# Kernel tuning notes

Hardware: AMD Instinct MI355X
Metric: run time of the kernel (lower is better)

The kernel has to match this reference:

```python
import jax, jax.numpy as jnp
import numpy as np

ALPHA = 0.9
EPS = 1e-5
SEQ, BATCH, D_MODEL, FF_DIM = 2048, 16, 512, 2048


def _layer_norm(x, g, b):
    m = jnp.mean(x, axis=-1, keepdims=True)
    v = jnp.mean((x - m) ** 2, axis=-1, keepdims=True)
    return (x - m) * jax.lax.rsqrt(v + EPS) * g + b


def _decay_matrix(seq, dtype):
    # Closed form of the torch roll/flip/tril loop:
    #   W[i, j] = alpha^{i-j+1}            for j <= i
    #   W[i, i] += 1 - sum_{k=1}^{i+1} alpha^k   (diag correction)
    i = jnp.arange(seq)
    diff = i[:, None] - i[None, :]                       # [S, S]
    causal = diff >= 0
    expo = jnp.where(causal, diff + 1, 0).astype(dtype)
    W = jnp.where(causal, jnp.asarray(ALPHA, dtype) ** expo, 0.0)
    W = W + jnp.diag(1.0 - W.sum(axis=1))
    return W


def setup_inputs() -> dict:
    key = jax.random.key(0)
    ks = jax.random.split(key, 8)
    s = lambda fan: 1.0 / np.sqrt(fan)
    return {
        "x": jax.random.normal(ks[0], (SEQ, BATCH, D_MODEL), jnp.float32),
        "w_lin": jax.random.normal(ks[1], (D_MODEL, D_MODEL), jnp.float32) * s(D_MODEL),
        "b_lin": jax.random.normal(ks[2], (D_MODEL,), jnp.float32) * 0.01,
        "w1": jax.random.normal(ks[3], (FF_DIM, D_MODEL), jnp.float32) * s(D_MODEL),
        "b1": jax.random.normal(ks[4], (FF_DIM,), jnp.float32) * 0.01,
        "w2": jax.random.normal(ks[5], (D_MODEL, FF_DIM), jnp.float32) * s(FF_DIM),
        "b2": jax.random.normal(ks[6], (D_MODEL,), jnp.float32) * 0.01,
        "g1": jnp.ones((D_MODEL,), jnp.float32),
        "beta1": jnp.zeros((D_MODEL,), jnp.float32),
        "g2": jnp.ones((D_MODEL,), jnp.float32),
        "beta2": jnp.zeros((D_MODEL,), jnp.float32),
    }


def reference(x, w_lin, b_lin, w1, b1, w2, b2, g1, beta1, g2, beta2):
    seq = x.shape[0]
    W = _decay_matrix(seq, x.dtype)                      # [S, S]

    # attention sublayer (dropout = identity in eval)
    y = _layer_norm(x, g1, beta1)
    z = jnp.einsum("sbd,ed->sbe", y, w_lin) + b_lin       # projection
    attn = jnp.einsum("ih,hbd->ibd", W, z)                # causal exp-decay mixing
    x = x + attn

    # feed-forward sublayer
    y = _layer_norm(x, g2, beta2)
    h = jax.nn.relu(jnp.einsum("sbd,fd->sbf", y, w1) + b1)
    ff = jnp.einsum("sbf,df->sbd", h, w2) + b2
    return x + ff
```

## Files before the change

### kernel.cpp

```cpp
#include <hip/hip_runtime.h>

#define SEQ 2048
#define BATCH 16
#define DMODEL 512
#define FFDIM 2048
#define NTOK (SEQ * BATCH)
#define ALPHA 0.9f

typedef unsigned short u16;
typedef __attribute__((ext_vector_type(8))) short short8;
typedef __attribute__((ext_vector_type(4))) float f32x4;

__device__ __forceinline__ float bf2f(u16 u) {
    unsigned int v = ((unsigned int)u) << 16;
    return __builtin_bit_cast(float, v);
}
__device__ __forceinline__ u16 f2bf(float f) {
    unsigned int v = __builtin_bit_cast(unsigned int, f);
    v += 0x7fffu + ((v >> 16) & 1u);
    return (u16)(v >> 16);
}

__global__ __launch_bounds__(256) void cvt_kernel(const float* __restrict__ in,
                                                  u16* __restrict__ out, int n) {
    const int i = (blockIdx.x * 256 + threadIdx.x) * 4;
    if (i >= n) return;
    float4 v = *(const float4*)(in + i);
    ushort4 o;
    o.x = f2bf(v.x); o.y = f2bf(v.y); o.z = f2bf(v.z); o.w = f2bf(v.w);
    *(ushort4*)(out + i) = o;
}

__global__ __launch_bounds__(256) void ln_kernel(const float* __restrict__ xin,
                                                 const float* __restrict__ g,
                                                 const float* __restrict__ b,
                                                 u16* __restrict__ y) {
    const int lane = threadIdx.x & 63;
    const int wave = threadIdx.x >> 6;
    const long tok = (long)blockIdx.x * 4 + wave;
    const long off = tok * DMODEL + lane * 8;

    float f[8];
    {
        const float4* xp = (const float4*)(xin + off);
        float4 a = xp[0], c = xp[1];
        f[0] = a.x; f[1] = a.y; f[2] = a.z; f[3] = a.w;
        f[4] = c.x; f[5] = c.y; f[6] = c.z; f[7] = c.w;
    }
    float s = 0.f, s2 = 0.f;
#pragma unroll
    for (int i = 0; i < 8; i++) { s += f[i]; s2 += f[i] * f[i]; }
#pragma unroll
    for (int o = 32; o > 0; o >>= 1) {
        s += __shfl_xor(s, o, 64);
        s2 += __shfl_xor(s2, o, 64);
    }
    const float mean = s * (1.f / DMODEL);
    const float var = s2 * (1.f / DMODEL) - mean * mean;
    const float inv = rsqrtf(var + 1e-5f);

    const float4* gp = (const float4*)(g + lane * 8);
    const float4* bp = (const float4*)(b + lane * 8);
    float4 g0 = gp[0], g1 = gp[1], b0 = bp[0], b1 = bp[1];
    float gg[8] = {g0.x, g0.y, g0.z, g0.w, g1.x, g1.y, g1.z, g1.w};
    float bb[8] = {b0.x, b0.y, b0.z, b0.w, b1.x, b1.y, b1.z, b1.w};
    short8 ov;
#pragma unroll
    for (int i = 0; i < 8; i++)
        ov[i] = (short)f2bf((f[i] - mean) * inv * gg[i] + bb[i]);
    *(short8*)(y + off) = ov;
}

#define SCAN_L 128
#define SCAN_H 160
__global__ __launch_bounds__(256) void scan_kernel(const u16* __restrict__ z,
                                                   const float* __restrict__ x,
                                                   float* __restrict__ x1) {
    const int p = blockIdx.x * 256 + threadIdx.x;
    const int s0 = blockIdx.y * SCAN_L;
    int s = s0 - SCAN_H;
    if (s < 0) s = 0;
    float r = 0.f;
    for (; s < s0; ++s)
        r = ALPHA * (bf2f(z[(long)s * 8192 + p]) + r);

    float ap = powf(ALPHA, (float)(s0 + 2));
#pragma unroll 4
    for (int i = 0; i < SCAN_L; i++) {
        const long idx = (long)(s0 + i) * 8192 + p;
        const float zf = bf2f(z[idx]);
        r = ALPHA * (zf + r);
        const float c = 1.f - (ALPHA - ap) * 10.f;
        x1[idx] = x[idx] + r + c * zf;
        ap *= ALPHA;
    }
}

#define BM 128
#define BN 128
#define BKK 64

typedef __attribute__((address_space(1))) unsigned int as1_u32;
typedef __attribute__((address_space(3))) unsigned int as3_u32;

__device__ __forceinline__ void gld_lds16(const void* g, const void* l) {
    __builtin_amdgcn_global_load_lds((as1_u32*)(unsigned long long)g,
                                     (as3_u32*)(unsigned int)(unsigned long long)l,
                                     16, 0, 0);
}

template <int EPI, bool OUT_F32>
__global__ __launch_bounds__(256, 2) void gemm128(const u16* __restrict__ A,
                                                  const u16* __restrict__ Bt,
                                                  const float* __restrict__ bias,
                                                  const float* __restrict__ resid,
                                                  void* __restrict__ C,
                                                  int M, int N, int K) {
    __shared__ alignas(16) u16 sA[2][BM * BKK];
    __shared__ alignas(16) u16 sB[2][BN * BKK];

    const int tid = threadIdx.x;
    const int lane = tid & 63;
    const int wave = tid >> 6;
    const int wr = wave >> 1;
    const int wc = wave & 1;
    const int l15 = lane & 15, q16 = lane >> 4;

    const int gx = gridDim.x;
    const int nwg = gx * gridDim.y;
    const int lin = blockIdx.y * gx + blockIdx.x;
    const int cpx = nwg >> 3;
    const int swz = (lin & 7) * cpx + (lin >> 3);
    const int m0 = (swz % gx) * BM;
    const int n0 = (swz / gx) * BN;

    const u16* gA[4];
    const u16* gB[4];
    int ldsoff[4];
#pragma unroll
    for (int i = 0; i < 4; i++) {
        const int ch = tid + i * 256;
        const int r = ch >> 3;
        const int oo = (ch & 7) ^ (r & 7);
        gA[i] = A + (long)(m0 + r) * K + oo * 8;
        gB[i] = Bt + (long)(n0 + r) * K + oo * 8;
        ldsoff[i] = ch * 8;
    }

    const int x7 = l15 & 7;
    int octk[2];
    octk[0] = ((0 + q16) ^ x7) * 8;
    octk[1] = ((4 + q16) ^ x7) * 8;
    const int rowA0 = wr * 64 + l15;
    const int rowB0 = wc * 64 + l15;

    f32x4 acc[4][4];
#pragma unroll
    for (int i = 0; i < 4; i++)
#pragma unroll
        for (int j = 0; j < 4; j++) acc[i][j] = (f32x4){0.f, 0.f, 0.f, 0.f};

    const int NT = K / BKK;

#pragma unroll
    for (int i = 0; i < 4; i++) gld_lds16(gA[i], &sA[0][ldsoff[i]]);
#pragma unroll
    for (int i = 0; i < 4; i++) gld_lds16(gB[i], &sB[0][ldsoff[i]]);

#pragma unroll 1
    for (int t = 0; t < NT; ++t) {
        const int pb = t & 1;
        if (t + 1 < NT) {
            const int pn = (t + 1) & 1;
            const int ko = (t + 1) * BKK;
#pragma unroll
            for (int i = 0; i < 4; i++) gld_lds16(gA[i] + ko, &sA[pn][ldsoff[i]]);
#pragma unroll
            for (int i = 0; i < 4; i++) gld_lds16(gB[i] + ko, &sB[pn][ldsoff[i]]);
            asm volatile("s_waitcnt vmcnt(8)" ::: "memory");
        } else {
            asm volatile("s_waitcnt vmcnt(0)" ::: "memory");
        }
        __builtin_amdgcn_s_barrier();

        const u16* pa = &sA[pb][rowA0 * BKK];
        const u16* pbb = &sB[pb][rowB0 * BKK];

#pragma unroll
        for (int kk = 0; kk < 2; kk++) {
            short8 a[4], b[4];
#pragma unroll
            for (int i = 0; i < 4; i++)
                a[i] = *(const short8*)(pa + i * 16 * BKK + octk[kk]);
#pragma unroll
            for (int j = 0; j < 4; j++)
                b[j] = *(const short8*)(pbb + j * 16 * BKK + octk[kk]);
#pragma unroll
            for (int i = 0; i < 4; i++)
#pragma unroll
                for (int j = 0; j < 4; j++)
                    acc[i][j] = __builtin_amdgcn_mfma_f32_16x16x32_bf16(a[i], b[j],
                                                                        acc[i][j], 0, 0, 0);
        }
        __builtin_amdgcn_s_barrier();
    }

#pragma unroll
    for (int i = 0; i < 4; i++) {
        const int row0 = m0 + wr * 64 + i * 16 + q16 * 4;
#pragma unroll
        for (int j = 0; j < 4; j++) {
            const int col = n0 + wc * 64 + j * 16 + l15;
            const float bv = bias[col];
#pragma unroll
            for (int r = 0; r < 4; r++) {
                const long idx = (long)(row0 + r) * N + col;
                float v = acc[i][j][r] + bv;
                if (EPI == 1) v = fmaxf(v, 0.f);
                if (EPI == 2) v += resid[idx];
                if (OUT_F32)
                    ((float*)C)[idx] = v;
                else
                    ((u16*)C)[idx] = f2bf(v);
            }
        }
    }
}

extern "C" void kernel_launch(void* const* d_in, const int* in_sizes, int n_in,
                              void* d_out, int out_size, void* d_ws, size_t ws_size,
                              hipStream_t stream) {
    const float* x = (const float*)d_in[0];
    const float* w_lin = (const float*)d_in[1];
    const float* b_lin = (const float*)d_in[2];
    const float* w1 = (const float*)d_in[3];
    const float* b1 = (const float*)d_in[4];
    const float* w2 = (const float*)d_in[5];
    const float* b2 = (const float*)d_in[6];
    const float* g1 = (const float*)d_in[7];
    const float* be1 = (const float*)d_in[8];
    const float* g2 = (const float*)d_in[9];
    const float* be2 = (const float*)d_in[10];
    float* out = (float*)d_out;

    char* ws = (char*)d_ws;
    const size_t MB = 1024 * 1024;
    u16* y = (u16*)(ws);
    float* x1 = (float*)(ws + 32 * MB);
    u16* h = (u16*)(ws + 96 * MB);
    u16* z = h;
    u16* wb_lin = (u16*)(ws + 224 * MB);
    u16* wb1 = (u16*)(ws + 225 * MB);
    u16* wb2 = (u16*)(ws + 228 * MB);

    cvt_kernel<<<(DMODEL * DMODEL) / 1024, 256, 0, stream>>>(w_lin, wb_lin, DMODEL * DMODEL);
    cvt_kernel<<<(FFDIM * DMODEL) / 1024, 256, 0, stream>>>(w1, wb1, FFDIM * DMODEL);
    cvt_kernel<<<(DMODEL * FFDIM) / 1024, 256, 0, stream>>>(w2, wb2, DMODEL * FFDIM);

    ln_kernel<<<NTOK / 4, 256, 0, stream>>>(x, g1, be1, y);
    gemm128<0, false><<<dim3(NTOK / BM, DMODEL / BN), 256, 0, stream>>>(y, wb_lin, b_lin, nullptr,
                                                                       z, NTOK, DMODEL, DMODEL);
    scan_kernel<<<dim3(BATCH * DMODEL / 256, SEQ / SCAN_L), 256, 0, stream>>>(z, x, x1);
    ln_kernel<<<NTOK / 4, 256, 0, stream>>>(x1, g2, be2, y);
    gemm128<1, false><<<dim3(NTOK / BM, FFDIM / BN), 256, 0, stream>>>(y, wb1, b1, nullptr, h,
                                                                      NTOK, FFDIM, DMODEL);
    gemm128<2, true><<<dim3(NTOK / BM, DMODEL / BN), 256, 0, stream>>>(h, wb2, b2, x1, out,
                                                                      NTOK, DMODEL, FFDIM);
}
```

Before: 456.6 us.

## Fuse decay scan with second LayerNorm and reorder GEMM tile swizzle

Merges the exponential-decay scan and the second LayerNorm into one kernel. Each block now owns one batch row's full 512-wide vector, processes two columns per thread, and does a block reduction per sequence step, so x1 is not re-read by a separate LN pass. The scan loop also gains 4-deep register prefetching of z and x. Separately, the GEMM workgroup-to-tile mapping is switched to an N-fastest order to change L2 reuse. The cost is a barrier per time step inside the scan, and the grid shrinks to 16x16 blocks, which may hurt latency hiding.

```diff
diff --git a/kernel.cpp b/kernel.cpp
--- a/kernel.cpp
+++ b/kernel.cpp
@@ -8,6 +8,7 @@
 #define ALPHA 0.9f
 
 typedef unsigned short u16;
+typedef unsigned int u32;
 typedef __attribute__((ext_vector_type(8))) short short8;
 typedef __attribute__((ext_vector_type(4))) float f32x4;
 
@@ -73,26 +74,88 @@
 
 #define SCAN_L 128
 #define SCAN_H 160
-__global__ __launch_bounds__(256) void scan_kernel(const u16* __restrict__ z,
-                                                   const float* __restrict__ x,
-                                                   float* __restrict__ x1) {
-    const int p = blockIdx.x * 256 + threadIdx.x;
+__global__ __launch_bounds__(256) void scan_ln_kernel(const u16* __restrict__ z,
+                                                      const float* __restrict__ x,
+                                                      const float* __restrict__ g,
+                                                      const float* __restrict__ be,
+                                                      float* __restrict__ x1,
+                                                      u16* __restrict__ y) {
+    __shared__ float red[2][4][2];
+    const int t = threadIdx.x;
+    const int lane = t & 63, wave = t >> 6;
+    const int b = blockIdx.x;
     const int s0 = blockIdx.y * SCAN_L;
-    int s = s0 - SCAN_H;
-    if (s < 0) s = 0;
-    float r = 0.f;
-    for (; s < s0; ++s)
-        r = ALPHA * (bf2f(z[(long)s * 8192 + p]) + r);
-
+    const int d0 = 2 * t;
+
+    const u32* zp = (const u32*)z;
+    const float2* xp = (const float2*)x;
+    float2* x1p = (float2*)x1;
+    u32* yp = (u32*)y;
+    const int colu = b * 256 + t;
+
+    const float gg0 = g[d0], gg1 = g[d0 + 1];
+    const float bb0 = be[d0], bb1 = be[d0 + 1];
+
+    float r0 = 0.f, r1 = 0.f;
+    {
+        int s = s0 - SCAN_H;
+        if (s < 0) s = 0;
+        for (; s < s0; ++s) {
+            const u32 zz = zp[(long)s * 4096 + colu];
+            r0 = ALPHA * (bf2f((u16)(zz & 0xffffu)) + r0);
+            r1 = ALPHA * (bf2f((u16)(zz >> 16)) + r1);
+        }
+    }
     float ap = powf(ALPHA, (float)(s0 + 2));
+
+    u32 zq[4];
+    float2 xq[4];
+#pragma unroll
+    for (int j = 0; j < 4; j++) {
+        zq[j] = zp[(long)(s0 + j) * 4096 + colu];
+        xq[j] = xp[(long)(s0 + j) * 4096 + colu];
+    }
+
 #pragma unroll 4
     for (int i = 0; i < SCAN_L; i++) {
-        const long idx = (long)(s0 + i) * 8192 + p;
-        const float zf = bf2f(z[idx]);
-        r = ALPHA * (zf + r);
+        const int sl = i & 3;
+        const u32 zz = zq[sl];
+        const float2 xx = xq[sl];
+        if (i + 4 < SCAN_L) {
+            zq[sl] = zp[(long)(s0 + i + 4) * 4096 + colu];
+            xq[sl] = xp[(long)(s0 + i + 4) * 4096 + colu];
+        }
+        const float z0 = bf2f((u16)(zz & 0xffffu));
+        const float z1 = bf2f((u16)(zz >> 16));
+        r0 = ALPHA * (z0 + r0);
+        r1 = ALPHA * (z1 + r1);
         const float c = 1.f - (ALPHA - ap) * 10.f;
-        x1[idx] = x[idx] + r + c * zf;
         ap *= ALPHA;
+        const float v0 = xx.x + r0 + c * z0;
+        const float v1 = xx.y + r1 + c * z1;
+        x1p[(long)(s0 + i) * 4096 + colu] = (float2){v0, v1};
+
+        float s1 = v0 + v1, s2 = v0 * v0 + v1 * v1;
+#pragma unroll
+        for (int o = 32; o > 0; o >>= 1) {
+            s1 += __shfl_xor(s1, o, 64);
+            s2 += __shfl_xor(s2, o, 64);
+        }
+        const int slot = i & 1;
+        if (lane == 0) {
+            red[slot][wave][0] = s1;
+            red[slot][wave][1] = s2;
+        }
+        asm volatile("s_waitcnt lgkmcnt(0)" ::: "memory");
+        __builtin_amdgcn_s_barrier();
+        const float S = red[slot][0][0] + red[slot][1][0] + red[slot][2][0] + red[slot][3][0];
+        const float S2 = red[slot][0][1] + red[slot][1][1] + red[slot][2][1] + red[slot][3][1];
+        const float mean = S * (1.f / DMODEL);
+        const float var = S2 * (1.f / DMODEL) - mean * mean;
+        const float inv = rsqrtf(var + 1e-5f);
+        const u16 o0 = f2bf((v0 - mean) * inv * gg0 + bb0);
+        const u16 o1 = f2bf((v1 - mean) * inv * gg1 + bb1);
+        yp[(long)(s0 + i) * 4096 + colu] = ((u32)o1 << 16) | (u32)o0;
     }
 }
 
@@ -126,13 +189,13 @@
     const int wc = wave & 1;
     const int l15 = lane & 15, q16 = lane >> 4;
 
-    const int gx = gridDim.x;
-    const int nwg = gx * gridDim.y;
-    const int lin = blockIdx.y * gx + blockIdx.x;
+    const int gy = gridDim.y;
+    const int nwg = gridDim.x * gy;
+    const int lin = blockIdx.x * gy + blockIdx.y;
     const int cpx = nwg >> 3;
     const int swz = (lin & 7) * cpx + (lin >> 3);
-    const int m0 = (swz % gx) * BM;
-    const int n0 = (swz / gx) * BN;
+    const int m0 = (swz / gy) * BM;
+    const int n0 = (swz % gy) * BN;
 
     const u16* gA[4];
     const u16* gB[4];
@@ -260,8 +323,7 @@
     ln_kernel<<<NTOK / 4, 256, 0, stream>>>(x, g1, be1, y);
     gemm128<0, false><<<dim3(NTOK / BM, DMODEL / BN), 256, 0, stream>>>(y, wb_lin, b_lin, nullptr,
                                                                        z, NTOK, DMODEL, DMODEL);
-    scan_kernel<<<dim3(BATCH * DMODEL / 256, SEQ / SCAN_L), 256, 0, stream>>>(z, x, x1);
-    ln_kernel<<<NTOK / 4, 256, 0, stream>>>(x1, g2, be2, y);
+    scan_ln_kernel<<<dim3(BATCH, SEQ / SCAN_L), 256, 0, stream>>>(z, x, g2, be2, x1, y);
     gemm128<1, false><<<dim3(NTOK / BM, FFDIM / BN), 256, 0, stream>>>(y, wb1, b1, nullptr, h,
                                                                       NTOK, FFDIM, DMODEL);
     gemm128<2, true><<<dim3(NTOK / BM, DMODEL / BN), 256, 0, stream>>>(h, wb2, b2, x1, out,
```

After: 506.0 us. 1.11x slower.

## Vectorize and prefetch scan over column pairs, shrink chunks, remap GEMM tile order

Applied to the files above, without the earlier changes.

The decay scan now handles two adjacent columns per thread, using 32-bit bf16-pair loads and float2 loads and stores, and keeps a 4-deep register prefetch queue so load latency overlaps the serial recurrence. The chunk length and warm-up halo are shortened (64/128), which gives more parallel blocks. The cost is more redundant warm-up work per output. The GEMM workgroup swizzle now assigns tiles M-major with N as the fast index, so neighbouring workgroups share A tiles in cache.

```diff
diff --git a/kernel.cpp b/kernel.cpp
--- a/kernel.cpp
+++ b/kernel.cpp
@@ -8,6 +8,7 @@
 #define ALPHA 0.9f
 
 typedef unsigned short u16;
+typedef unsigned int u32;
 typedef __attribute__((ext_vector_type(8))) short short8;
 typedef __attribute__((ext_vector_type(4))) float f32x4;
 
@@ -71,28 +72,67 @@
     *(short8*)(y + off) = ov;
 }
 
-#define SCAN_L 128
-#define SCAN_H 160
+#define SCAN_L 64
+#define SCAN_H 128
+#define NCOLU (BATCH * DMODEL / 2)
 __global__ __launch_bounds__(256) void scan_kernel(const u16* __restrict__ z,
                                                    const float* __restrict__ x,
                                                    float* __restrict__ x1) {
-    const int p = blockIdx.x * 256 + threadIdx.x;
+    const int colu = blockIdx.x * 256 + threadIdx.x;
     const int s0 = blockIdx.y * SCAN_L;
-    int s = s0 - SCAN_H;
-    if (s < 0) s = 0;
-    float r = 0.f;
-    for (; s < s0; ++s)
-        r = ALPHA * (bf2f(z[(long)s * 8192 + p]) + r);
+
+    const u32* zp = (const u32*)z;
+    const float2* xp = (const float2*)x;
+    float2* x1p = (float2*)x1;
+
+    float r0 = 0.f, r1 = 0.f;
+
+    {
+        int sb = s0 - SCAN_H;
+        if (sb < 0) sb = 0;
+        const int nw = s0 - sb;
+        if (nw > 0) {
+            u32 zq[4];
+#pragma unroll
+            for (int j = 0; j < 4; j++) zq[j] = zp[(long)(sb + j) * NCOLU + colu];
+            for (int i = 0; i < nw; i += 4) {
+#pragma unroll
+                for (int j = 0; j < 4; j++) {
+                    const u32 zz = zq[j];
+                    if (i + j + 4 < nw)
+                        zq[j] = zp[(long)(sb + i + j + 4) * NCOLU + colu];
+                    r0 = ALPHA * (bf2f((u16)(zz & 0xffffu)) + r0);
+                    r1 = ALPHA * (bf2f((u16)(zz >> 16)) + r1);
+                }
+            }
+        }
+    }
 
     float ap = powf(ALPHA, (float)(s0 + 2));
+
+    u32 zq[4];
+    float2 xq[4];
+#pragma unroll
+    for (int j = 0; j < 4; j++) {
+        zq[j] = zp[(long)(s0 + j) * NCOLU + colu];
+        xq[j] = xp[(long)(s0 + j) * NCOLU + colu];
+    }
 #pragma unroll 4
     for (int i = 0; i < SCAN_L; i++) {
-        const long idx = (long)(s0 + i) * 8192 + p;
-        const float zf = bf2f(z[idx]);
-        r = ALPHA * (zf + r);
+        const int sl = i & 3;
+        const u32 zz = zq[sl];
+        const float2 xx = xq[sl];
+        if (i + 4 < SCAN_L) {
+            zq[sl] = zp[(long)(s0 + i + 4) * NCOLU + colu];
+            xq[sl] = xp[(long)(s0 + i + 4) * NCOLU + colu];
+        }
+        const float z0 = bf2f((u16)(zz & 0xffffu));
+        const float z1 = bf2f((u16)(zz >> 16));
+        r0 = ALPHA * (z0 + r0);
+        r1 = ALPHA * (z1 + r1);
         const float c = 1.f - (ALPHA - ap) * 10.f;
-        x1[idx] = x[idx] + r + c * zf;
         ap *= ALPHA;
+        x1p[(long)(s0 + i) * NCOLU + colu] = (float2){xx.x + r0 + c * z0, xx.y + r1 + c * z1};
     }
 }
 
@@ -126,13 +166,12 @@
     const int wc = wave & 1;
     const int l15 = lane & 15, q16 = lane >> 4;
 
-    const int gx = gridDim.x;
-    const int nwg = gx * gridDim.y;
-    const int lin = blockIdx.y * gx + blockIdx.x;
-    const int cpx = nwg >> 3;
-    const int swz = (lin & 7) * cpx + (lin >> 3);
-    const int m0 = (swz % gx) * BM;
-    const int n0 = (swz / gx) * BN;
+    const int gy = gridDim.y;
+    const int nwg = gridDim.x * gy;
+    const int d = blockIdx.y * gridDim.x + blockIdx.x;
+    const int wgid = (d & 7) * (nwg >> 3) + (d >> 3);
+    const int m0 = (wgid / gy) * BM;
+    const int n0 = (wgid % gy) * BN;
 
     const u16* gA[4];
     const u16* gB[4];
@@ -260,7 +299,7 @@
     ln_kernel<<<NTOK / 4, 256, 0, stream>>>(x, g1, be1, y);
     gemm128<0, false><<<dim3(NTOK / BM, DMODEL / BN), 256, 0, stream>>>(y, wb_lin, b_lin, nullptr,
                                                                        z, NTOK, DMODEL, DMODEL);
-    scan_kernel<<<dim3(BATCH * DMODEL / 256, SEQ / SCAN_L), 256, 0, stream>>>(z, x, x1);
+    scan_kernel<<<dim3(NCOLU / 256, SEQ / SCAN_L), 256, 0, stream>>>(z, x, x1);
     ln_kernel<<<NTOK / 4, 256, 0, stream>>>(x1, g2, be2, y);
     gemm128<1, false><<<dim3(NTOK / BM, FFDIM / BN), 256, 0, stream>>>(y, wb1, b1, nullptr, h,
                                                                       NTOK, FFDIM, DMODEL);
```

Measured after the change: 437.4 us. 4.2% less time.
